# Kernel tuning notes

Measured on AMD Instinct MI355X. Metric: run time of the kernel, lower is better.

## Reference

```python
import jax, jax.numpy as jnp
import numpy as np

BLKPT = 1.0     # black-point percentile
WHTPT = 99.0    # white-point percentile
MAX_MULT = 1.5  # cap on brightening multiplier


def setup_inputs() -> dict:
    key = jax.random.key(0)
    # [B, 3, H, W] image in [0, 1]
    image = jax.random.uniform(key, (16, 3, 1024, 1024), dtype=jnp.float32)
    # standard BT.601 RGB->YUV matrix (module buffer RGB2YUV)
    rgb2yuv = jnp.array([[0.299, 0.587, 0.114],
                         [-0.14713, -0.28886, 0.436],
                         [0.615, -0.51499, -0.10001]], dtype=jnp.float32)
    return {"image": image, "rgb2yuv": rgb2yuv}


def reference(image, rgb2yuv):
    # Only the Y (luma) channel of the YUV conversion is consumed, so we
    # contract with the first matrix row instead of materializing full YUV.
    y = jnp.einsum('j,bjhw->bhw', rgb2yuv[0], image)        # [B, H, W]
    yf = y.reshape(y.shape[0], -1)                          # [B, H*W]
    blkpt = jnp.percentile(yf, BLKPT, axis=1)               # [B]
    whtpt = jnp.percentile(yf, WHTPT, axis=1)               # [B]
    mult = jnp.minimum(1.0 / (whtpt - blkpt), MAX_MULT)     # max_mult > 0 branch
    blkpt = blkpt[:, None, None, None]
    mult = mult[:, None, None, None]
    return jnp.clip((image - blkpt) * mult, 0.0, 1.0)
```

## Files before the change

kernel.cpp:

```cpp
#include <hip/hip_runtime.h>
#include <hip/hip_bf16.h>

#define NPIX (1024 * 1024)
#define NBATCH 16
#define NBINS 8192

__global__ void hist_kernel(const float* __restrict__ img,
                            const float* __restrict__ rgb2yuv,
                            unsigned int* __restrict__ block_hist,
                            int subPerBatch) {
    __shared__ unsigned int lh[NBINS];
    for (int i = threadIdx.x; i < NBINS; i += blockDim.x) lh[i] = 0;
    const float c0 = rgb2yuv[0];
    const float c1 = rgb2yuv[1];
    const float c2 = rgb2yuv[2];
    __syncthreads();

    const int b = blockIdx.x / subPerBatch;
    const int s = blockIdx.x % subPerBatch;
    const int pixPerBlock = NPIX / subPerBatch;
    const size_t base = (size_t)b * 3 * NPIX + (size_t)s * pixPerBlock;

    const float4* r4 = (const float4*)(img + base);
    const float4* g4 = (const float4*)(img + base + NPIX);
    const float4* b4 = (const float4*)(img + base + 2 * (size_t)NPIX);
    const int n4 = pixPerBlock / 4;

    const float scale = (float)NBINS;
    for (int i = threadIdx.x; i < n4; i += blockDim.x) {
        float4 R = r4[i];
        float4 G = g4[i];
        float4 B = b4[i];
        float y0 = c0 * R.x + c1 * G.x + c2 * B.x;
        float y1 = c0 * R.y + c1 * G.y + c2 * B.y;
        float y2 = c0 * R.z + c1 * G.z + c2 * B.z;
        float y3 = c0 * R.w + c1 * G.w + c2 * B.w;
        int i0 = min(NBINS - 1, max(0, (int)(y0 * scale)));
        int i1 = min(NBINS - 1, max(0, (int)(y1 * scale)));
        int i2 = min(NBINS - 1, max(0, (int)(y2 * scale)));
        int i3 = min(NBINS - 1, max(0, (int)(y3 * scale)));
        atomicAdd(&lh[i0], 1u);
        atomicAdd(&lh[i1], 1u);
        atomicAdd(&lh[i2], 1u);
        atomicAdd(&lh[i3], 1u);
    }
    __syncthreads();

    unsigned int* dst = block_hist + (size_t)blockIdx.x * NBINS;
    for (int i = threadIdx.x; i < NBINS; i += blockDim.x) dst[i] = lh[i];
}

__global__ __launch_bounds__(1024) void scan_kernel(
        const unsigned int* __restrict__ block_hist,
        float* __restrict__ stats, int subPerBatch) {
    __shared__ unsigned int hist[NBINS];
    __shared__ unsigned int segsum[1024];
    __shared__ float vals[4];

    const int b = blockIdx.x;
    const int t = threadIdx.x;

    for (int i = t; i < NBINS; i += 1024) {
        unsigned int s = 0;
        const unsigned int* p = block_hist + ((size_t)b * subPerBatch) * NBINS + i;
        for (int k = 0; k < subPerBatch; ++k) s += p[(size_t)k * NBINS];
        hist[i] = s;
    }
    __syncthreads();

    const int BPT = NBINS / 1024;
    unsigned int ss = 0;
#pragma unroll
    for (int j = 0; j < BPT; ++j) ss += hist[t * BPT + j];
    segsum[t] = ss;
    __syncthreads();

    for (int off = 1; off < 1024; off <<= 1) {
        unsigned int v = segsum[t];
        unsigned int add = (t >= off) ? segsum[t - off] : 0u;
        __syncthreads();
        segsum[t] = v + add;
        __syncthreads();
    }

    const unsigned int cumincl = segsum[t];
    const unsigned int cumbefore = (t > 0) ? segsum[t - 1] : 0u;

    const unsigned int ranks[4] = {10485u, 10486u, 1038089u, 1038090u};
#pragma unroll
    for (int q = 0; q < 4; ++q) {
        unsigned int r = ranks[q];
        if (r >= cumbefore && r < cumincl) {
            unsigned int running = cumbefore;
#pragma unroll
            for (int j = 0; j < BPT; ++j) {
                unsigned int c = hist[t * BPT + j];
                if (r < running + c) {
                    float v = ((float)(t * BPT + j) +
                               ((float)(r - running) + 0.5f) / (float)c) *
                              (1.0f / (float)NBINS);
                    vals[q] = v;
                    break;
                }
                running += c;
            }
        }
    }
    __syncthreads();

    if (t == 0) {
        float blk = 0.25f * vals[0] + 0.75f * vals[1];
        float wht = 0.75f * vals[2] + 0.25f * vals[3];
        float mult = fminf(1.0f / (wht - blk), 1.5f);
        stats[b * 2 + 0] = blk;
        stats[b * 2 + 1] = mult;
    }
}

__global__ void apply_kernel(const float* __restrict__ img,
                             const float* __restrict__ stats,
                             float* __restrict__ out) {
    const int blocksPerBatch = (3 * NPIX / 4) / 1024;
    const int b = blockIdx.x / blocksPerBatch;
    const int c = blockIdx.x % blocksPerBatch;
    const float blk = stats[b * 2 + 0];
    const float mult = stats[b * 2 + 1];

    const float4* in4 = (const float4*)(img + (size_t)b * 3 * NPIX) + (size_t)c * 1024;
    float4* out4 = (float4*)(out + (size_t)b * 3 * NPIX) + (size_t)c * 1024;

#pragma unroll
    for (int i = 0; i < 4; ++i) {
        int idx = i * 256 + threadIdx.x;
        float4 v = in4[idx];
        v.x = fminf(fmaxf((v.x - blk) * mult, 0.0f), 1.0f);
        v.y = fminf(fmaxf((v.y - blk) * mult, 0.0f), 1.0f);
        v.z = fminf(fmaxf((v.z - blk) * mult, 0.0f), 1.0f);
        v.w = fminf(fmaxf((v.w - blk) * mult, 0.0f), 1.0f);
        out4[idx] = v;
    }
}

extern "C" void kernel_launch(void* const* d_in, const int* in_sizes, int n_in,
                              void* d_out, int out_size, void* d_ws, size_t ws_size,
                              hipStream_t stream) {
    const float* img = (const float*)d_in[0];
    const float* rgb2yuv = (const float*)d_in[1];
    float* out = (float*)d_out;

    float* stats = (float*)d_ws;
    unsigned int* block_hist = (unsigned int*)((char*)d_ws + 256);

    int subPerBatch = 32;
    while (subPerBatch > 1 &&
           256 + (size_t)subPerBatch * NBATCH * NBINS * 4 > ws_size) {
        subPerBatch >>= 1;
    }

    hist_kernel<<<NBATCH * subPerBatch, 256, 0, stream>>>(img, rgb2yuv, block_hist,
                                                          subPerBatch);
    scan_kernel<<<NBATCH, 1024, 0, stream>>>(block_hist, stats, subPerBatch);

    const int applyBlocks = NBATCH * ((3 * NPIX / 4) / 1024);
    apply_kernel<<<applyBlocks, 256, 0, stream>>>(img, stats, out);
}
```

Baseline: 410.6 us.

## Merge per-block histograms with global atomics and double histogram block count

```diff
diff --git a/kernel.cpp b/kernel.cpp
--- a/kernel.cpp
+++ b/kernel.cpp
@@ -4,11 +4,18 @@
 #define NPIX (1024 * 1024)
 #define NBATCH 16
 #define NBINS 8192
+#define SUBPB 64
 
-__global__ void hist_kernel(const float* __restrict__ img,
-                            const float* __restrict__ rgb2yuv,
-                            unsigned int* __restrict__ block_hist,
-                            int subPerBatch) {
+__global__ void zero_kernel(unsigned int* __restrict__ ghist) {
+    int i = blockIdx.x * blockDim.x + threadIdx.x;
+    int n = NBATCH * NBINS;
+    for (; i < n; i += gridDim.x * blockDim.x) ghist[i] = 0u;
+}
+
+__global__ __launch_bounds__(256) void hist_kernel(
+        const float* __restrict__ img,
+        const float* __restrict__ rgb2yuv,
+        unsigned int* __restrict__ ghist) {
     __shared__ unsigned int lh[NBINS];
     for (int i = threadIdx.x; i < NBINS; i += blockDim.x) lh[i] = 0;
     const float c0 = rgb2yuv[0];
@@ -16,9 +23,9 @@
     const float c2 = rgb2yuv[2];
     __syncthreads();
 
-    const int b = blockIdx.x / subPerBatch;
-    const int s = blockIdx.x % subPerBatch;
-    const int pixPerBlock = NPIX / subPerBatch;
+    const int b = blockIdx.x / SUBPB;
+    const int s = blockIdx.x % SUBPB;
+    const int pixPerBlock = NPIX / SUBPB;
     const size_t base = (size_t)b * 3 * NPIX + (size_t)s * pixPerBlock;
 
     const float4* r4 = (const float4*)(img + base);
@@ -46,13 +53,16 @@
     }
     __syncthreads();
 
-    unsigned int* dst = block_hist + (size_t)blockIdx.x * NBINS;
-    for (int i = threadIdx.x; i < NBINS; i += blockDim.x) dst[i] = lh[i];
+    unsigned int* dst = ghist + (size_t)b * NBINS;
+    for (int i = threadIdx.x; i < NBINS; i += blockDim.x) {
+        unsigned int v = lh[i];
+        if (v) atomicAdd(&dst[i], v);
+    }
 }
 
 __global__ __launch_bounds__(1024) void scan_kernel(
-        const unsigned int* __restrict__ block_hist,
-        float* __restrict__ stats, int subPerBatch) {
+        const unsigned int* __restrict__ ghist,
+        float* __restrict__ stats) {
     __shared__ unsigned int hist[NBINS];
     __shared__ unsigned int segsum[1024];
     __shared__ float vals[4];
@@ -60,12 +70,8 @@
     const int b = blockIdx.x;
     const int t = threadIdx.x;
 
-    for (int i = t; i < NBINS; i += 1024) {
-        unsigned int s = 0;
-        const unsigned int* p = block_hist + ((size_t)b * subPerBatch) * NBINS + i;
-        for (int k = 0; k < subPerBatch; ++k) s += p[(size_t)k * NBINS];
-        hist[i] = s;
-    }
+    for (int i = t; i < NBINS; i += 1024)
+        hist[i] = ghist[(size_t)b * NBINS + i];
     __syncthreads();
 
     const int BPT = NBINS / 1024;
@@ -117,9 +123,10 @@
     }
 }
 
-__global__ void apply_kernel(const float* __restrict__ img,
-                             const float* __restrict__ stats,
-                             float* __restrict__ out) {
+__global__ __launch_bounds__(256) void apply_kernel(
+        const float* __restrict__ img,
+        const float* __restrict__ stats,
+        float* __restrict__ out) {
     const int blocksPerBatch = (3 * NPIX / 4) / 1024;
     const int b = blockIdx.x / blocksPerBatch;
     const int c = blockIdx.x % blocksPerBatch;
@@ -149,17 +156,11 @@
     float* out = (float*)d_out;
 
     float* stats = (float*)d_ws;
-    unsigned int* block_hist = (unsigned int*)((char*)d_ws + 256);
+    unsigned int* ghist = (unsigned int*)((char*)d_ws + 256);
 
-    int subPerBatch = 32;
-    while (subPerBatch > 1 &&
-           256 + (size_t)subPerBatch * NBATCH * NBINS * 4 > ws_size) {
-        subPerBatch >>= 1;
-    }
-
-    hist_kernel<<<NBATCH * subPerBatch, 256, 0, stream>>>(img, rgb2yuv, block_hist,
-                                                          subPerBatch);
-    scan_kernel<<<NBATCH, 1024, 0, stream>>>(block_hist, stats, subPerBatch);
+    zero_kernel<<<64, 256, 0, stream>>>(ghist);
+    hist_kernel<<<NBATCH * SUBPB, 256, 0, stream>>>(img, rgb2yuv, ghist);
+    scan_kernel<<<NBATCH, 1024, 0, stream>>>(ghist, stats);
 
     const int applyBlocks = NBATCH * ((3 * NPIX / 4) / 1024);
     apply_kernel<<<applyBlocks, 256, 0, stream>>>(img, stats, out);
```

After: 383.0 us. 1.07x faster.
